# Optimization experiments

Measured on AMD Instinct MI355X. Metric: run time of the kernel, lower is better.

Reference implementation:

```python
import jax, jax.numpy as jnp
import numpy as np

B, A, D, CIN = 256, 512, 64, 4  # batch, action_dim, day_length, in channels
C1, C2 = 4, 16
EPS = 1e-5


def _ln(x):
    # non-affine LayerNorm over (C, H, W), per-sample
    m = jnp.mean(x, axis=(1, 2, 3), keepdims=True)
    v = jnp.var(x, axis=(1, 2, 3), keepdims=True)
    return (x - m) / jnp.sqrt(v + EPS)


def _dblock(x, w_dil, w_pw):
    # dilated (1,3) conv, dilation 2, padding (0,2) -> width preserved
    y = jax.lax.conv_general_dilated(
        x, w_dil, window_strides=(1, 1), padding=[(0, 0), (2, 2)],
        rhs_dilation=(2, 2), dimension_numbers=('NCHW', 'OIHW', 'NCHW'))
    y = _ln(y)
    y = jnp.einsum('bchw,oc->bohw', y, w_pw[:, :, 0, 0])  # 1x1 conv
    return jax.nn.gelu(y, approximate=False)


def setup_inputs() -> dict:
    key = jax.random.key(0)
    ks = jax.random.split(key, 11)
    f = lambda k, shp: (jax.random.normal(k, shp, dtype=jnp.float32) * 0.1)
    return {
        's': jax.random.normal(ks[0], (B, A, D, CIN), dtype=jnp.float32),
        'w': jax.random.normal(ks[1], (B, A), dtype=jnp.float32),
        'd1w1': f(ks[2], (C1, CIN, 1, 3)),
        'd1w2': f(ks[3], (C1, C1, 1, 1)),
        'd2w1': f(ks[4], (C1, CIN, 1, 3)),
        'd2w2': f(ks[5], (C1, C1, 1, 1)),
        'd3w1': f(ks[6], (C1, CIN, 1, 3)),
        'd3w2': f(ks[7], (C1, C1, 1, 1)),
        'cw': f(ks[8], (C1, 3 * C1, 1, 1)),
        'c2w': f(ks[9], (C2, C1, 1, D)),
        'c3w': f(ks[10], (1, C2 + 1, 1, 1)),
    }


def reference(s, w, d1w1, d1w2, d2w1, d2w2, d3w1, d3w2, cw, c2w, c3w):
    s = jnp.transpose(s, (0, 3, 1, 2))          # [B, 4, A, D]
    x1 = _dblock(s, d1w1, d1w2)
    x2 = _dblock(s + x1, d2w1, d2w2)
    x3 = _dblock(s + x1 + x2, d3w1, d3w2)
    x = jnp.concatenate([x1, x2, x3], axis=1)   # [B, 12, A, D]
    x = _ln(x)
    x = jnp.einsum('bchw,oc->bohw', x, cw[:, :, 0, 0])      # 1x1 conv -> [B,4,A,D]
    x = jnp.einsum('bchw,ocw->boh', x, c2w[:, :, 0, :])[..., None]  # (1,D) conv -> [B,16,A,1]
    x = _ln(x)
    x = jnp.concatenate([x, w[:, None, :, None]], axis=1)   # [B,17,A,1]
    x = jnp.einsum('bchw,oc->bohw', x, c3w[:, :, 0, 0])     # [B,1,A,1]
    x = _ln(x)
    return x[:, 0, :, 0]                                    # [B, A]
```

## Files before the change

kernel.cpp:

```cpp
#include <hip/hip_runtime.h>
#include <math.h>


#define EPS_LN 1e-5f
typedef float4 f4;

__device__ __forceinline__ float gelu_f(float v) {
    return 0.5f * v * (1.0f + erff(v * 0.70710678118654752440f));
}

__device__ __forceinline__ void conv4(const f4 a, const f4 c, const f4 e,
                                      const float* __restrict__ wd, float y[4]) {
#pragma unroll
    for (int o = 0; o < 4; ++o) {
        const float* wv = wd + o * 12;
        y[o] = fmaf(a.x, wv[0], fmaf(c.x, wv[1], fmaf(e.x, wv[2],
               fmaf(a.y, wv[3], fmaf(c.y, wv[4], fmaf(e.y, wv[5],
               fmaf(a.z, wv[6], fmaf(c.z, wv[7], fmaf(e.z, wv[8],
               fmaf(a.w, wv[9], fmaf(c.w, wv[10], e.w * wv[11])))))))))));
    }
}

__device__ __forceinline__ void block_red2(float& a, float& b2, float* red,
                                           float* bc, int tid) {
#pragma unroll
    for (int off = 32; off > 0; off >>= 1) {
        a  += __shfl_down(a,  off, 64);
        b2 += __shfl_down(b2, off, 64);
    }
    if ((tid & 63) == 0) { red[tid >> 6] = a; red[8 + (tid >> 6)] = b2; }
    __syncthreads();
    if (tid == 0) {
        float x = 0.f, y = 0.f;
#pragma unroll
        for (int i = 0; i < 8; ++i) { x += red[i]; y += red[8 + i]; }
        bc[0] = x; bc[1] = y;
    }
    __syncthreads();
    a = bc[0]; b2 = bc[1];
}

__global__ __launch_bounds__(512)
void tcn_fused(const float* __restrict__ sIn, const float* __restrict__ wIn,
               const float* __restrict__ w1d, const float* __restrict__ w1p,
               const float* __restrict__ w2d, const float* __restrict__ w2p,
               const float* __restrict__ w3d, const float* __restrict__ w3p,
               const float* __restrict__ cw,  const float* __restrict__ c2w,
               const float* __restrict__ c3w, float* __restrict__ out,
               f4* __restrict__ baseT) {
    const int b   = blockIdx.x;
    const int tid = threadIdx.x;

    __shared__ float red[16];
    __shared__ float bc[2];
    __shared__ float Klds[16];

    if (tid < 16) {
        float k = 0.f;
        for (int co = 0; co < 4; ++co) {
            float cs = 0.f;
            for (int j = 0; j < 12; ++j) cs += cw[co * 12 + j];
            const float* p = c2w + tid * 256 + co * 64;
            float t = 0.f;
            for (int d = 0; d < 64; ++d) t += p[d];
            k = fmaf(cs, t, k);
        }
        Klds[tid] = k;
    }

    const f4* s4 = (const f4*)sIn;
    const size_t srow = ((size_t)b * 512 + tid) * 64;
    const size_t brow = (size_t)b * (64 * 512) + tid;
    const f4 z4 = make_float4(0.f, 0.f, 0.f, 0.f);
    const float NY = 4.f * 512.f * 64.f;

    float s1 = 0.f, s2 = 0.f;
    {
        f4 wA = z4, wB = z4, wC = s4[srow], wD = s4[srow + 1], wE;
        for (int d = 0; d < 64; ++d) {
            wE = (d + 2 < 64) ? s4[srow + d + 2] : z4;
            float y[4]; conv4(wA, wC, wE, w1d, y);
#pragma unroll
            for (int o = 0; o < 4; ++o) { s1 += y[o]; s2 = fmaf(y[o], y[o], s2); }
            wA = wB; wB = wC; wC = wD; wD = wE;
        }
    }
    block_red2(s1, s2, red, bc, tid);
    float m1 = s1 / NY;
    float r1 = rsqrtf(s2 / NY - m1 * m1 + EPS_LN);

    float t16a[16];
#pragma unroll
    for (int o = 0; o < 16; ++o) t16a[o] = 0.f;
    float cs1 = 0.f, cs2 = 0.f;

    float q1 = 0.f, q2 = 0.f;
    {
        f4 wA = z4, wB = z4, wC = s4[srow], wD = s4[srow + 1], wE;
        f4 bA = z4, bB = z4, bC = z4, bD = z4, bE;
        for (int d = 0; d < 66; ++d) {
            if (d < 64) {
                wE = (d + 2 < 64) ? s4[srow + d + 2] : z4;
                float y[4]; conv4(wA, wC, wE, w1d, y);
#pragma unroll
                for (int o = 0; o < 4; ++o) y[o] = (y[o] - m1) * r1;
                float g[4];
#pragma unroll
                for (int o = 0; o < 4; ++o) {
                    float zz = fmaf(y[0], w1p[o*4+0], fmaf(y[1], w1p[o*4+1],
                               fmaf(y[2], w1p[o*4+2], y[3] * w1p[o*4+3])));
                    g[o] = gelu_f(zz);
                }
#pragma unroll
                for (int o = 0; o < 4; ++o) { cs1 += g[o]; cs2 = fmaf(g[o], g[o], cs2); }
                float u[4];
#pragma unroll
                for (int co = 0; co < 4; ++co)
                    u[co] = fmaf(g[0], cw[co*12+0], fmaf(g[1], cw[co*12+1],
                            fmaf(g[2], cw[co*12+2], g[3] * cw[co*12+3])));
#pragma unroll
                for (int o = 0; o < 16; ++o) {
                    const float* p = c2w + o * 256 + d;
                    t16a[o] = fmaf(u[0], p[0], fmaf(u[1], p[64],
                              fmaf(u[2], p[128], fmaf(u[3], p[192], t16a[o]))));
                }
                f4 nb;
                nb.x = wC.x + g[0]; nb.y = wC.y + g[1];
                nb.z = wC.z + g[2]; nb.w = wC.w + g[3];
                baseT[brow + (size_t)d * 512] = nb;
                bE = nb;
                wA = wB; wB = wC; wC = wD; wD = wE;
            } else bE = z4;
            if (d >= 2) {
                float y2[4]; conv4(bA, bC, bE, w2d, y2);
#pragma unroll
                for (int o = 0; o < 4; ++o) { q1 += y2[o]; q2 = fmaf(y2[o], y2[o], q2); }
            }
            bA = bB; bB = bC; bC = bD; bD = bE;
        }
    }
    block_red2(q1, q2, red, bc, tid);
    float m2s = q1 / NY;
    float r2s = rsqrtf(q2 / NY - m2s * m2s + EPS_LN);

    float q31 = 0.f, q32 = 0.f;
    {
        f4 gA = z4, gB = z4, gC = z4, gD = z4, gE;
        f4 hA = z4, hB = z4, hC = z4, hD = z4, hE;
        for (int t = 0; t < 68; ++t) {
            gE = (t < 64) ? baseT[brow + (size_t)t * 512] : z4;
            if (t >= 2 && t < 66) {
                const int e = t - 2;
                float y[4]; conv4(gA, gC, gE, w2d, y);
#pragma unroll
                for (int o = 0; o < 4; ++o) y[o] = (y[o] - m2s) * r2s;
                float g[4];
#pragma unroll
                for (int o = 0; o < 4; ++o) {
                    float zz = fmaf(y[0], w2p[o*4+0], fmaf(y[1], w2p[o*4+1],
                               fmaf(y[2], w2p[o*4+2], y[3] * w2p[o*4+3])));
                    g[o] = gelu_f(zz);
                }
#pragma unroll
                for (int o = 0; o < 4; ++o) { cs1 += g[o]; cs2 = fmaf(g[o], g[o], cs2); }
                float u[4];
#pragma unroll
                for (int co = 0; co < 4; ++co)
                    u[co] = fmaf(g[0], cw[co*12+4], fmaf(g[1], cw[co*12+5],
                            fmaf(g[2], cw[co*12+6], g[3] * cw[co*12+7])));
#pragma unroll
                for (int o = 0; o < 16; ++o) {
                    const float* p = c2w + o * 256 + e;
                    t16a[o] = fmaf(u[0], p[0], fmaf(u[1], p[64],
                              fmaf(u[2], p[128], fmaf(u[3], p[192], t16a[o]))));
                }
                f4 nb;
                nb.x = gC.x + g[0]; nb.y = gC.y + g[1];
                nb.z = gC.z + g[2]; nb.w = gC.w + g[3];
                baseT[brow + (size_t)e * 512] = nb;
                hE = nb;
            } else hE = z4;
            if (t >= 4) {
                float y3[4]; conv4(hA, hC, hE, w3d, y3);
#pragma unroll
                for (int o = 0; o < 4; ++o) { q31 += y3[o]; q32 = fmaf(y3[o], y3[o], q32); }
            }
            gA = gB; gB = gC; gC = gD; gD = gE;
            hA = hB; hB = hC; hC = hD; hD = hE;
        }
    }
    block_red2(q31, q32, red, bc, tid);
    float m3s = q31 / NY;
    float r3s = rsqrtf(q32 / NY - m3s * m3s + EPS_LN);

    {
        f4 wA = z4, wB = z4, wC = baseT[brow], wD = baseT[brow + 512], wE;
        for (int d = 0; d < 64; ++d) {
            wE = (d + 2 < 64) ? baseT[brow + (size_t)(d + 2) * 512] : z4;
            float y[4]; conv4(wA, wC, wE, w3d, y);
#pragma unroll
            for (int o = 0; o < 4; ++o) y[o] = (y[o] - m3s) * r3s;
            float g[4];
#pragma unroll
            for (int o = 0; o < 4; ++o) {
                float zz = fmaf(y[0], w3p[o*4+0], fmaf(y[1], w3p[o*4+1],
                           fmaf(y[2], w3p[o*4+2], y[3] * w3p[o*4+3])));
                g[o] = gelu_f(zz);
            }
#pragma unroll
            for (int o = 0; o < 4; ++o) { cs1 += g[o]; cs2 = fmaf(g[o], g[o], cs2); }
            float u[4];
#pragma unroll
            for (int co = 0; co < 4; ++co)
                u[co] = fmaf(g[0], cw[co*12+8], fmaf(g[1], cw[co*12+9],
                        fmaf(g[2], cw[co*12+10], g[3] * cw[co*12+11])));
#pragma unroll
            for (int o = 0; o < 16; ++o) {
                const float* p = c2w + o * 256 + d;
                t16a[o] = fmaf(u[0], p[0], fmaf(u[1], p[64],
                          fmaf(u[2], p[128], fmaf(u[3], p[192], t16a[o]))));
            }
            wA = wB; wB = wC; wC = wD; wD = wE;
        }
    }

    block_red2(cs1, cs2, red, bc, tid);
    const float NC = 12.f * 512.f * 64.f;
    float mcat = cs1 / NC;
    float rcat = rsqrtf(cs2 / NC - mcat * mcat + EPS_LN);

    float tv[16];
    float p1 = 0.f, p2 = 0.f;
#pragma unroll
    for (int o = 0; o < 16; ++o) {
        float v = rcat * (t16a[o] - mcat * Klds[o]);
        tv[o] = v; p1 += v; p2 = fmaf(v, v, p2);
    }
    block_red2(p1, p2, red, bc, tid);
    const float N16 = 16.f * 512.f;
    float m16 = p1 / N16;
    float r16 = rsqrtf(p2 / N16 - m16 * m16 + EPS_LN);

    float v = wIn[(size_t)b * 512 + tid] * c3w[16];
#pragma unroll
    for (int o = 0; o < 16; ++o) v = fmaf((tv[o] - m16) * r16, c3w[o], v);
    float f1 = v, f2 = v * v;
    block_red2(f1, f2, red, bc, tid);
    float mA = f1 / 512.f;
    float rA = rsqrtf(f2 / 512.f - mA * mA + EPS_LN);

    out[(size_t)b * 512 + tid] = (v - mA) * rA;
}

extern "C" void kernel_launch(void* const* d_in, const int* in_sizes, int n_in,
                              void* d_out, int out_size, void* d_ws, size_t ws_size,
                              hipStream_t stream) {
    const float* s   = (const float*)d_in[0];
    const float* w   = (const float*)d_in[1];
    const float* w1d = (const float*)d_in[2];
    const float* w1p = (const float*)d_in[3];
    const float* w2d = (const float*)d_in[4];
    const float* w2p = (const float*)d_in[5];
    const float* w3d = (const float*)d_in[6];
    const float* w3p = (const float*)d_in[7];
    const float* cw  = (const float*)d_in[8];
    const float* c2w = (const float*)d_in[9];
    const float* c3w = (const float*)d_in[10];
    tcn_fused<<<dim3(256), dim3(512), 0, stream>>>(
        s, w, w1d, w1p, w2d, w2p, w3d, w3p, cw, c2w, c3w,
        (float*)d_out, (f4*)d_ws);
}
```

Baseline: 532.1 us.

## Split day dimension across two thread halves with LDS halo exchange

Doubles the block to 1024 threads, with each half handling 32 of the 64 day positions for each action row. Halo values at the split boundary go through shared memory after a block barrier, and the two halves' partial c2w accumulators are combined through LDS before the final norms. The fused two-stage pipelined loops are replaced by separate stats and apply passes per block, which adds global re-reads of the intermediate buffer. The aim is more parallelism per block to hide latency on a grid of only 256 blocks, at the cost of extra syncs, redundant conv recomputation and larger LDS use.

Result: slower. 818.7 us (+53.9%).

```diff
diff --git a/kernel.cpp b/kernel.cpp
--- a/kernel.cpp
+++ b/kernel.cpp
@@ -28,19 +28,47 @@
         a  += __shfl_down(a,  off, 64);
         b2 += __shfl_down(b2, off, 64);
     }
-    if ((tid & 63) == 0) { red[tid >> 6] = a; red[8 + (tid >> 6)] = b2; }
+    if ((tid & 63) == 0) { red[tid >> 6] = a; red[16 + (tid >> 6)] = b2; }
     __syncthreads();
     if (tid == 0) {
         float x = 0.f, y = 0.f;
 #pragma unroll
-        for (int i = 0; i < 8; ++i) { x += red[i]; y += red[8 + i]; }
+        for (int i = 0; i < 16; ++i) { x += red[i]; y += red[16 + i]; }
         bc[0] = x; bc[1] = y;
     }
     __syncthreads();
     a = bc[0]; b2 = bc[1];
 }
 
-__global__ __launch_bounds__(512)
+__device__ __forceinline__ void pw_accum(const float y[4], float r, float c,
+    const float* __restrict__ wp, const float* __restrict__ cw, int cwo,
+    const float* __restrict__ c2w, int d,
+    float& cs1, float& cs2, float* t16a, float g[4]) {
+    float yn[4];
+#pragma unroll
+    for (int o = 0; o < 4; ++o) yn[o] = fmaf(y[o], r, c);
+#pragma unroll
+    for (int o = 0; o < 4; ++o) {
+        float zz = fmaf(yn[0], wp[o*4+0], fmaf(yn[1], wp[o*4+1],
+                   fmaf(yn[2], wp[o*4+2], yn[3] * wp[o*4+3])));
+        g[o] = gelu_f(zz);
+    }
+#pragma unroll
+    for (int o = 0; o < 4; ++o) { cs1 += g[o]; cs2 = fmaf(g[o], g[o], cs2); }
+    float u[4];
+#pragma unroll
+    for (int co = 0; co < 4; ++co)
+        u[co] = fmaf(g[0], cw[co*12+cwo+0], fmaf(g[1], cw[co*12+cwo+1],
+                fmaf(g[2], cw[co*12+cwo+2], g[3] * cw[co*12+cwo+3])));
+#pragma unroll
+    for (int o = 0; o < 16; ++o) {
+        const float* p = c2w + o * 256 + d;
+        t16a[o] = fmaf(u[0], p[0], fmaf(u[1], p[64],
+                  fmaf(u[2], p[128], fmaf(u[3], p[192], t16a[o]))));
+    }
+}
+
+__global__ __launch_bounds__(1024)
 void tcn_fused(const float* __restrict__ sIn, const float* __restrict__ wIn,
                const float* __restrict__ w1d, const float* __restrict__ w1p,
                const float* __restrict__ w2d, const float* __restrict__ w2p,
@@ -50,35 +78,59 @@
                f4* __restrict__ baseT) {
     const int b   = blockIdx.x;
     const int tid = threadIdx.x;
-
-    __shared__ float red[16];
+    const int a   = tid & 511;
+    const int h   = tid >> 9;
+    const int Dlo = h << 5;
+
+    __shared__ float red[32];
     __shared__ float bc[2];
     __shared__ float Klds[16];
+    __shared__ f4 haloA[512][2][2];
+    __shared__ f4 haloB[512][2][2];
+    __shared__ float t16p[512][17];
 
     if (tid < 16) {
         float k = 0.f;
         for (int co = 0; co < 4; ++co) {
-            float cs = 0.f;
-            for (int j = 0; j < 12; ++j) cs += cw[co * 12 + j];
+            float csum = 0.f;
+            for (int j = 0; j < 12; ++j) csum += cw[co * 12 + j];
             const float* p = c2w + tid * 256 + co * 64;
             float t = 0.f;
             for (int d = 0; d < 64; ++d) t += p[d];
-            k = fmaf(cs, t, k);
+            k = fmaf(csum, t, k);
         }
         Klds[tid] = k;
     }
 
-    const f4* s4 = (const f4*)sIn;
-    const size_t srow = ((size_t)b * 512 + tid) * 64;
-    const size_t brow = (size_t)b * (64 * 512) + tid;
+    const f4* srow = (const f4*)sIn + ((size_t)b * 512 + a) * 64;
+    f4* brow = baseT + (size_t)b * (64 * 512) + a;
     const f4 z4 = make_float4(0.f, 0.f, 0.f, 0.f);
     const float NY = 4.f * 512.f * 64.f;
 
+    auto ldS = [&](int d) -> f4 { return ((unsigned)d < 64u) ? srow[d] : z4; };
+    auto ldB2 = [&](int d) -> f4 {
+        if (d >= Dlo && d < Dlo + 32) return brow[(size_t)d * 512];
+        if (h) { if (d == 30) return haloA[a][0][0];
+                 if (d == 31) return haloA[a][0][1]; }
+        else   { if (d == 32) return haloA[a][1][0];
+                 if (d == 33) return haloA[a][1][1]; }
+        return z4;
+    };
+    auto ldB3 = [&](int d) -> f4 {
+        if (d >= Dlo && d < Dlo + 32) return brow[(size_t)d * 512];
+        if (h) { if (d == 30) return haloB[a][0][0];
+                 if (d == 31) return haloB[a][0][1]; }
+        else   { if (d == 32) return haloB[a][1][0];
+                 if (d == 33) return haloB[a][1][1]; }
+        return z4;
+    };
+
     float s1 = 0.f, s2 = 0.f;
     {
-        f4 wA = z4, wB = z4, wC = s4[srow], wD = s4[srow + 1], wE;
-        for (int d = 0; d < 64; ++d) {
-            wE = (d + 2 < 64) ? s4[srow + d + 2] : z4;
+        f4 wA = ldS(Dlo - 2), wB = ldS(Dlo - 1), wC = ldS(Dlo), wD = ldS(Dlo + 1), wE;
+        for (int i = 0; i < 32; ++i) {
+            const int d = Dlo + i;
+            wE = ldS(d + 2);
             float y[4]; conv4(wA, wC, wE, w1d, y);
 #pragma unroll
             for (int o = 0; o < 4; ++o) { s1 += y[o]; s2 = fmaf(y[o], y[o], s2); }
@@ -88,142 +140,105 @@
     block_red2(s1, s2, red, bc, tid);
     float m1 = s1 / NY;
     float r1 = rsqrtf(s2 / NY - m1 * m1 + EPS_LN);
+    float c1n = -m1 * r1;
 
     float t16a[16];
 #pragma unroll
     for (int o = 0; o < 16; ++o) t16a[o] = 0.f;
     float cs1 = 0.f, cs2 = 0.f;
 
+    {
+        const int cap0 = h ? Dlo : Dlo + 30;
+        f4 capA0 = z4, capA1 = z4;
+        f4 wA = ldS(Dlo - 2), wB = ldS(Dlo - 1), wC = ldS(Dlo), wD = ldS(Dlo + 1), wE;
+        for (int i = 0; i < 32; ++i) {
+            const int d = Dlo + i;
+            wE = ldS(d + 2);
+            float y[4]; conv4(wA, wC, wE, w1d, y);
+            float g[4];
+            pw_accum(y, r1, c1n, w1p, cw, 0, c2w, d, cs1, cs2, t16a, g);
+            f4 nb;
+            nb.x = wC.x + g[0]; nb.y = wC.y + g[1];
+            nb.z = wC.z + g[2]; nb.w = wC.w + g[3];
+            brow[(size_t)d * 512] = nb;
+            if (d == cap0) capA0 = nb; else if (d == cap0 + 1) capA1 = nb;
+            wA = wB; wB = wC; wC = wD; wD = wE;
+        }
+        haloA[a][h][0] = capA0; haloA[a][h][1] = capA1;
+    }
+    __syncthreads();
+
     float q1 = 0.f, q2 = 0.f;
     {
-        f4 wA = z4, wB = z4, wC = s4[srow], wD = s4[srow + 1], wE;
-        f4 bA = z4, bB = z4, bC = z4, bD = z4, bE;
-        for (int d = 0; d < 66; ++d) {
-            if (d < 64) {
-                wE = (d + 2 < 64) ? s4[srow + d + 2] : z4;
-                float y[4]; conv4(wA, wC, wE, w1d, y);
-#pragma unroll
-                for (int o = 0; o < 4; ++o) y[o] = (y[o] - m1) * r1;
-                float g[4];
-#pragma unroll
-                for (int o = 0; o < 4; ++o) {
-                    float zz = fmaf(y[0], w1p[o*4+0], fmaf(y[1], w1p[o*4+1],
-                               fmaf(y[2], w1p[o*4+2], y[3] * w1p[o*4+3])));
-                    g[o] = gelu_f(zz);
-                }
-#pragma unroll
-                for (int o = 0; o < 4; ++o) { cs1 += g[o]; cs2 = fmaf(g[o], g[o], cs2); }
-                float u[4];
-#pragma unroll
-                for (int co = 0; co < 4; ++co)
-                    u[co] = fmaf(g[0], cw[co*12+0], fmaf(g[1], cw[co*12+1],
-                            fmaf(g[2], cw[co*12+2], g[3] * cw[co*12+3])));
-#pragma unroll
-                for (int o = 0; o < 16; ++o) {
-                    const float* p = c2w + o * 256 + d;
-                    t16a[o] = fmaf(u[0], p[0], fmaf(u[1], p[64],
-                              fmaf(u[2], p[128], fmaf(u[3], p[192], t16a[o]))));
-                }
-                f4 nb;
-                nb.x = wC.x + g[0]; nb.y = wC.y + g[1];
-                nb.z = wC.z + g[2]; nb.w = wC.w + g[3];
-                baseT[brow + (size_t)d * 512] = nb;
-                bE = nb;
-                wA = wB; wB = wC; wC = wD; wD = wE;
-            } else bE = z4;
-            if (d >= 2) {
-                float y2[4]; conv4(bA, bC, bE, w2d, y2);
-#pragma unroll
-                for (int o = 0; o < 4; ++o) { q1 += y2[o]; q2 = fmaf(y2[o], y2[o], q2); }
-            }
-            bA = bB; bB = bC; bC = bD; bD = bE;
+        f4 wA = ldB2(Dlo - 2), wB = ldB2(Dlo - 1), wC = ldB2(Dlo), wD = ldB2(Dlo + 1), wE;
+        for (int i = 0; i < 32; ++i) {
+            const int d = Dlo + i;
+            wE = ldB2(d + 2);
+            float y[4]; conv4(wA, wC, wE, w2d, y);
+#pragma unroll
+            for (int o = 0; o < 4; ++o) { q1 += y[o]; q2 = fmaf(y[o], y[o], q2); }
+            wA = wB; wB = wC; wC = wD; wD = wE;
         }
     }
     block_red2(q1, q2, red, bc, tid);
     float m2s = q1 / NY;
     float r2s = rsqrtf(q2 / NY - m2s * m2s + EPS_LN);
+    float c2n = -m2s * r2s;
+
+    {
+        const int cap0 = h ? Dlo : Dlo + 30;
+        f4 capB0 = z4, capB1 = z4;
+        f4 vA = ldB2(Dlo - 2), vB = ldB2(Dlo - 1), vC = ldB2(Dlo), vD = ldB2(Dlo + 1), vE;
+        for (int i = 0; i < 32; ++i) {
+            const int d = Dlo + i;
+            vE = ldB2(d + 2);
+            float y[4]; conv4(vA, vC, vE, w2d, y);
+            float g[4];
+            pw_accum(y, r2s, c2n, w2p, cw, 4, c2w, d, cs1, cs2, t16a, g);
+            f4 nb;
+            nb.x = vC.x + g[0]; nb.y = vC.y + g[1];
+            nb.z = vC.z + g[2]; nb.w = vC.w + g[3];
+            brow[(size_t)d * 512] = nb;
+            if (d == cap0) capB0 = nb; else if (d == cap0 + 1) capB1 = nb;
+            vA = vB; vB = vC; vC = vD; vD = vE;
+        }
+        haloB[a][h][0] = capB0; haloB[a][h][1] = capB1;
+    }
+    __syncthreads();
 
     float q31 = 0.f, q32 = 0.f;
     {
-        f4 gA = z4, gB = z4, gC = z4, gD = z4, gE;
-        f4 hA = z4, hB = z4, hC = z4, hD = z4, hE;
-        for (int t = 0; t < 68; ++t) {
-            gE = (t < 64) ? baseT[brow + (size_t)t * 512] : z4;
-            if (t >= 2 && t < 66) {
-                const int e = t - 2;
-                float y[4]; conv4(gA, gC, gE, w2d, y);
-#pragma unroll
-                for (int o = 0; o < 4; ++o) y[o] = (y[o] - m2s) * r2s;
-                float g[4];
-#pragma unroll
-                for (int o = 0; o < 4; ++o) {
-                    float zz = fmaf(y[0], w2p[o*4+0], fmaf(y[1], w2p[o*4+1],
-                               fmaf(y[2], w2p[o*4+2], y[3] * w2p[o*4+3])));
-                    g[o] = gelu_f(zz);
-                }
-#pragma unroll
-                for (int o = 0; o < 4; ++o) { cs1 += g[o]; cs2 = fmaf(g[o], g[o], cs2); }
-                float u[4];
-#pragma unroll
-                for (int co = 0; co < 4; ++co)
-                    u[co] = fmaf(g[0], cw[co*12+4], fmaf(g[1], cw[co*12+5],
-                            fmaf(g[2], cw[co*12+6], g[3] * cw[co*12+7])));
-#pragma unroll
-                for (int o = 0; o < 16; ++o) {
-                    const float* p = c2w + o * 256 + e;
-                    t16a[o] = fmaf(u[0], p[0], fmaf(u[1], p[64],
-                              fmaf(u[2], p[128], fmaf(u[3], p[192], t16a[o]))));
-                }
-                f4 nb;
-                nb.x = gC.x + g[0]; nb.y = gC.y + g[1];
-                nb.z = gC.z + g[2]; nb.w = gC.w + g[3];
-                baseT[brow + (size_t)e * 512] = nb;
-                hE = nb;
-            } else hE = z4;
-            if (t >= 4) {
-                float y3[4]; conv4(hA, hC, hE, w3d, y3);
-#pragma unroll
-                for (int o = 0; o < 4; ++o) { q31 += y3[o]; q32 = fmaf(y3[o], y3[o], q32); }
-            }
-            gA = gB; gB = gC; gC = gD; gD = gE;
-            hA = hB; hB = hC; hC = hD; hD = hE;
+        f4 wA = ldB3(Dlo - 2), wB = ldB3(Dlo - 1), wC = ldB3(Dlo), wD = ldB3(Dlo + 1), wE;
+        for (int i = 0; i < 32; ++i) {
+            const int d = Dlo + i;
+            wE = ldB3(d + 2);
+            float y[4]; conv4(wA, wC, wE, w3d, y);
+#pragma unroll
+            for (int o = 0; o < 4; ++o) { q31 += y[o]; q32 = fmaf(y[o], y[o], q32); }
+            wA = wB; wB = wC; wC = wD; wD = wE;
         }
     }
     block_red2(q31, q32, red, bc, tid);
     float m3s = q31 / NY;
     float r3s = rsqrtf(q32 / NY - m3s * m3s + EPS_LN);
-
-    {
-        f4 wA = z4, wB = z4, wC = baseT[brow], wD = baseT[brow + 512], wE;
-        for (int d = 0; d < 64; ++d) {
-            wE = (d + 2 < 64) ? baseT[brow + (size_t)(d + 2) * 512] : z4;
+    float c3n = -m3s * r3s;
+
+    {
+        f4 wA = ldB3(Dlo - 2), wB = ldB3(Dlo - 1), wC = ldB3(Dlo), wD = ldB3(Dlo + 1), wE;
+        for (int i = 0; i < 32; ++i) {
+            const int d = Dlo + i;
+            wE = ldB3(d + 2);
             float y[4]; conv4(wA, wC, wE, w3d, y);
-#pragma unroll
-            for (int o = 0; o < 4; ++o) y[o] = (y[o] - m3s) * r3s;
             float g[4];
-#pragma unroll
-            for (int o = 0; o < 4; ++o) {
-                float zz = fmaf(y[0], w3p[o*4+0], fmaf(y[1], w3p[o*4+1],
-                           fmaf(y[2], w3p[o*4+2], y[3] * w3p[o*4+3])));
-                g[o] = gelu_f(zz);
-            }
-#pragma unroll
-            for (int o = 0; o < 4; ++o) { cs1 += g[o]; cs2 = fmaf(g[o], g[o], cs2); }
-            float u[4];
-#pragma unroll
-            for (int co = 0; co < 4; ++co)
-                u[co] = fmaf(g[0], cw[co*12+8], fmaf(g[1], cw[co*12+9],
-                        fmaf(g[2], cw[co*12+10], g[3] * cw[co*12+11])));
-#pragma unroll
-            for (int o = 0; o < 16; ++o) {
-                const float* p = c2w + o * 256 + d;
-                t16a[o] = fmaf(u[0], p[0], fmaf(u[1], p[64],
-                          fmaf(u[2], p[128], fmaf(u[3], p[192], t16a[o]))));
-            }
-            wA = wB; wB = wC; wC = wD; wD = wE;
-        }
-    }
-
+            pw_accum(y, r3s, c3n, w3p, cw, 8, c2w, d, cs1, cs2, t16a, g);
+            wA = wB; wB = wC; wC = wD; wD = wE;
+        }
+    }
+
+    if (h == 1) {
+#pragma unroll
+        for (int o = 0; o < 16; ++o) t16p[a][o] = t16a[o];
+    }
     block_red2(cs1, cs2, red, bc, tid);
     const float NC = 12.f * 512.f * 64.f;
     float mcat = cs1 / NC;
@@ -231,25 +246,30 @@
 
     float tv[16];
     float p1 = 0.f, p2 = 0.f;
-#pragma unroll
-    for (int o = 0; o < 16; ++o) {
-        float v = rcat * (t16a[o] - mcat * Klds[o]);
-        tv[o] = v; p1 += v; p2 = fmaf(v, v, p2);
+    if (h == 0) {
+#pragma unroll
+        for (int o = 0; o < 16; ++o) {
+            float tot = t16a[o] + t16p[a][o];
+            float v = rcat * (tot - mcat * Klds[o]);
+            tv[o] = v; p1 += v; p2 = fmaf(v, v, p2);
+        }
     }
     block_red2(p1, p2, red, bc, tid);
     const float N16 = 16.f * 512.f;
     float m16 = p1 / N16;
     float r16 = rsqrtf(p2 / N16 - m16 * m16 + EPS_LN);
 
-    float v = wIn[(size_t)b * 512 + tid] * c3w[16];
-#pragma unroll
-    for (int o = 0; o < 16; ++o) v = fmaf((tv[o] - m16) * r16, c3w[o], v);
-    float f1 = v, f2 = v * v;
+    float v = 0.f, f1 = 0.f, f2 = 0.f;
+    if (h == 0) {
+        v = wIn[(size_t)b * 512 + a] * c3w[16];
+#pragma unroll
+        for (int o = 0; o < 16; ++o) v = fmaf((tv[o] - m16) * r16, c3w[o], v);
+        f1 = v; f2 = v * v;
+    }
     block_red2(f1, f2, red, bc, tid);
     float mA = f1 / 512.f;
     float rA = rsqrtf(f2 / 512.f - mA * mA + EPS_LN);
-
-    out[(size_t)b * 512 + tid] = (v - mA) * rA;
+    if (h == 0) out[(size_t)b * 512 + a] = (v - mA) * rA;
 }
 
 extern "C" void kernel_launch(void* const* d_in, const int* in_sizes, int n_in,
@@ -266,7 +286,7 @@
     const float* cw  = (const float*)d_in[8];
     const float* c2w = (const float*)d_in[9];
     const float* c3w = (const float*)d_in[10];
-    tcn_fused<<<dim3(256), dim3(512), 0, stream>>>(
+    tcn_fused<<<dim3(256), dim3(1024), 0, stream>>>(
         s, w, w1d, w1p, w2d, w2p, w3d, w3p, cw, c2w, c3w,
         (float*)d_out, (f4*)d_ws);
 }
```
